# Optimization experiments

Hardware: AMD Instinct MI355X
Metric: run time of the kernel (lower is better)

Reference implementation:

```python
import jax, jax.numpy as jnp
import numpy as np

NODE_DIM = 128
EDGE_DIM = 128
N_NODES = 50000
N_EDGES = 600000


def setup_inputs() -> dict:
    key = jax.random.key(0)
    ks = jax.random.split(key, 10)
    d, e = NODE_DIM, EDGE_DIM
    s = lambda fan_in: 1.0 / np.sqrt(fan_in)
    return {
        "x": jax.random.normal(ks[0], (N_NODES, d), dtype=jnp.float32),
        "edge_index": jax.random.randint(ks[1], (2, N_EDGES), 0, N_NODES, dtype=jnp.int64),
        "edge_attr": jax.random.normal(ks[2], (N_EDGES, e), dtype=jnp.float32),
        # edge_net: Linear(2d+e -> 2d), Softplus, Linear(2d -> d), Softplus
        "W1": jax.random.uniform(ks[3], (2 * d + e, 2 * d), jnp.float32, -s(2 * d + e), s(2 * d + e)),
        "b1": jax.random.uniform(ks[4], (2 * d,), jnp.float32, -s(2 * d + e), s(2 * d + e)),
        "W2": jax.random.uniform(ks[5], (2 * d, d), jnp.float32, -s(2 * d), s(2 * d)),
        "b2": jax.random.uniform(ks[6], (d,), jnp.float32, -s(2 * d), s(2 * d)),
        # node_net: Linear(2d -> d), Softplus
        "Wn": jax.random.uniform(ks[7], (2 * d, d), jnp.float32, -s(2 * d), s(2 * d)),
        "bn": jax.random.uniform(ks[8], (d,), jnp.float32, -s(2 * d), s(2 * d)),
    }


def reference(x, edge_index, edge_attr, W1, b1, W2, b2, Wn, bn):
    row, col = edge_index[0], edge_index[1]
    # gather node features per edge and concat with edge features
    edge_input = jnp.concatenate([x[row], x[col], edge_attr], axis=-1)  # [E, 2d+e]
    h = jax.nn.softplus(edge_input @ W1 + b1)  # [E, 2d]
    edge_emb = jax.nn.softplus(h @ W2 + b2)    # [E, d]
    # scatter-add messages to destination nodes
    aggr = jax.ops.segment_sum(edge_emb, col, num_segments=x.shape[0])  # [N, d]
    node_input = jnp.concatenate([x, aggr], axis=-1)  # [N, 2d]
    x_new = jax.nn.softplus(node_input @ Wn + bn)     # [N, d]
    return x_new + x
```

## Files before the change

### kernel.cpp

```cpp
#include <hip/hip_runtime.h>

#define EE 600000
#define NN 50000
#define DD 128

typedef __bf16 bf16x8 __attribute__((ext_vector_type(8)));
typedef float f32x4 __attribute__((ext_vector_type(4)));
typedef unsigned short u16x8 __attribute__((ext_vector_type(8)));

__device__ inline unsigned short f2bf(float f) {
  unsigned int u = __builtin_bit_cast(unsigned int, f);
  u += 0x7FFFu + ((u >> 16) & 1u);
  return (unsigned short)(u >> 16);
}

__device__ inline float softplus_f(float v) {
  return fmaxf(v, 0.0f) + __logf(1.0f + __expf(-fabsf(v)));
}

__global__ void prep_kernel(const float* __restrict__ x,
                            const float* __restrict__ W1, const float* __restrict__ W2,
                            const float* __restrict__ Wn,
                            unsigned short* __restrict__ xbf, unsigned short* __restrict__ w1f,
                            unsigned short* __restrict__ w2f, unsigned short* __restrict__ wnf) {
  const int id = blockIdx.x * 256 + threadIdx.x;
  if (id < 800000) {
    const f32x4* src = (const f32x4*)(x + (size_t)id * 8);
    f32x4 f0 = src[0], f1 = src[1];
    u16x8 v;
#pragma unroll
    for (int j = 0; j < 4; ++j) { v[j] = f2bf(f0[j]); v[4 + j] = f2bf(f1[j]); }
    *(u16x8*)(xbf + (size_t)id * 8) = v;
  } else if (id < 812288) {
    const int u = id - 800000;
    const int l = u & 63, t2 = u >> 6, nt = t2 & 15, kt = t2 >> 4;
    const int n = nt * 16 + (l & 15);
    const int kb = kt * 32 + ((l >> 4) << 3);
    u16x8 v;
#pragma unroll
    for (int j = 0; j < 8; ++j) v[j] = f2bf(W1[(size_t)(kb + j) * 256 + n]);
    *(u16x8*)(w1f + (size_t)u * 8) = v;
  } else if (id < 816384) {
    const int u = id - 812288;
    const int l = u & 63, t2 = u >> 6, nt = t2 & 7, kt = t2 >> 3;
    const int n = nt * 16 + (l & 15);
    const int kb = kt * 32 + ((l >> 4) << 3);
    u16x8 v;
#pragma unroll
    for (int j = 0; j < 8; ++j) v[j] = f2bf(W2[(size_t)(kb + j) * 128 + n]);
    *(u16x8*)(w2f + (size_t)u * 8) = v;
  } else if (id < 820480) {
    const int u = id - 816384;
    const int l = u & 63, t2 = u >> 6, nt = t2 & 7, kt = t2 >> 3;
    const int n = nt * 16 + (l & 15);
    const int kb = kt * 32 + ((l >> 4) << 3);
    u16x8 v;
#pragma unroll
    for (int j = 0; j < 8; ++j) v[j] = f2bf(Wn[(size_t)(kb + j) * 128 + n]);
    *(u16x8*)(wnf + (size_t)u * 8) = v;
  }
}

__global__ __launch_bounds__(256, 3) void edge_kernel(
    const int* __restrict__ ei, const float* __restrict__ eattr,
    const float* __restrict__ b1, const float* __restrict__ b2,
    const unsigned short* __restrict__ xbf,
    const unsigned short* __restrict__ w1f, const unsigned short* __restrict__ w2f,
    float* __restrict__ aggr) {
  __shared__ __align__(16) unsigned short At[24576];
  __shared__ int colS[64];
  const int t = threadIdx.x;
  const int lane = t & 63;
  const int w = t >> 6;
  const int base = blockIdx.x * 64;

  {
    const int r = t >> 2, p = t & 3;
    const int e = base + r;
    const int sr = ei[e], sc = ei[EE + e];
    if (p == 0) colS[r] = sc;
    const u16x8* xr = (const u16x8*)(xbf + (size_t)sr * DD + p * 32);
    const u16x8* xc = (const u16x8*)(xbf + (size_t)sc * DD + p * 32);
    const f32x4* ea = (const f32x4*)(eattr + (size_t)e * DD + p * 32);
    const int swz = (r & 7) << 4;
    unsigned short* rowp = At + ((r * 768) >> 1);
#pragma unroll
    for (int i = 0; i < 4; ++i) {
      const int c2 = (p * 32 + i * 8) * 2;
      *(u16x8*)(rowp + ((c2 ^ swz) >> 1)) = xr[i];
      *(u16x8*)(rowp + (((256 + c2) ^ swz) >> 1)) = xc[i];
      f32x4 f0 = ea[2 * i], f1 = ea[2 * i + 1];
      u16x8 v;
#pragma unroll
      for (int j = 0; j < 4; ++j) { v[j] = f2bf(f0[j]); v[4 + j] = f2bf(f1[j]); }
      *(u16x8*)(rowp + (((512 + c2) ^ swz) >> 1)) = v;
    }
  }
  __syncthreads();

  const int lr = lane & 15;
  const int lkb = ((lane >> 4) << 3) * 2;

  f32x4 acc[4][4] = {};
#pragma unroll
  for (int kt = 0; kt < 12; ++kt) {
    bf16x8 a[4];
#pragma unroll
    for (int mt = 0; mt < 4; ++mt) {
      const int row = mt * 16 + lr;
      const int cb = kt * 64 + lkb;
      a[mt] = __builtin_bit_cast(bf16x8,
              *(const u16x8*)(At + ((row * 768 + (cb ^ ((row & 7) << 4))) >> 1)));
    }
#pragma unroll
    for (int nt = 0; nt < 4; ++nt) {
      const u16x8 bv = *(const u16x8*)(w1f + ((size_t)((kt * 16 + (w * 4 + nt)) * 64 + lane) << 3));
      const bf16x8 b = __builtin_bit_cast(bf16x8, bv);
#pragma unroll
      for (int mt = 0; mt < 4; ++mt)
        acc[mt][nt] = __builtin_amdgcn_mfma_f32_16x16x32_bf16(a[mt], b, acc[mt][nt], 0, 0, 0);
    }
  }
  __syncthreads();

#pragma unroll
  for (int nt = 0; nt < 4; ++nt) {
    const int col = w * 64 + nt * 16 + lr;
    const float bias = b1[col];
#pragma unroll
    for (int mt = 0; mt < 4; ++mt) {
#pragma unroll
      for (int reg = 0; reg < 4; ++reg) {
        const int row = mt * 16 + ((lane >> 4) << 2) + reg;
        const float hv = softplus_f(acc[mt][nt][reg] + bias);
        At[(row * 512 + ((col * 2) ^ ((row & 7) << 4))) >> 1] = f2bf(hv);
      }
    }
  }
  __syncthreads();

  f32x4 acc2[4][2] = {};
#pragma unroll
  for (int kt = 0; kt < 8; ++kt) {
    bf16x8 a[4];
#pragma unroll
    for (int mt = 0; mt < 4; ++mt) {
      const int row = mt * 16 + lr;
      const int cb = kt * 64 + lkb;
      a[mt] = __builtin_bit_cast(bf16x8,
              *(const u16x8*)(At + ((row * 512 + (cb ^ ((row & 7) << 4))) >> 1)));
    }
#pragma unroll
    for (int nt = 0; nt < 2; ++nt) {
      const u16x8 bv = *(const u16x8*)(w2f + ((size_t)((kt * 8 + (w * 2 + nt)) * 64 + lane) << 3));
      const bf16x8 b = __builtin_bit_cast(bf16x8, bv);
#pragma unroll
      for (int mt = 0; mt < 4; ++mt)
        acc2[mt][nt] = __builtin_amdgcn_mfma_f32_16x16x32_bf16(a[mt], b, acc2[mt][nt], 0, 0, 0);
    }
  }

#pragma unroll
  for (int nt = 0; nt < 2; ++nt) {
    const int col = w * 32 + nt * 16 + lr;
    const float bias = b2[col];
#pragma unroll
    for (int mt = 0; mt < 4; ++mt) {
#pragma unroll
      for (int reg = 0; reg < 4; ++reg) {
        const int row = mt * 16 + ((lane >> 4) << 2) + reg;
        const float v = softplus_f(acc2[mt][nt][reg] + bias);
        float* p = aggr + (size_t)colS[row] * DD + col;
        __hip_atomic_fetch_add(p, v, __ATOMIC_RELAXED, __HIP_MEMORY_SCOPE_AGENT);
      }
    }
  }
}

__global__ __launch_bounds__(256, 4) void node_kernel(
    const float* __restrict__ x, const float* __restrict__ bn,
    const unsigned short* __restrict__ xbf, const unsigned short* __restrict__ wnf,
    const float* __restrict__ aggr, float* __restrict__ out) {
  __shared__ __align__(16) unsigned short At[16384];
  const int t = threadIdx.x;
  const int lane = t & 63;
  const int w = t >> 6;
  const int base = blockIdx.x * 64;

  {
    const int r = t >> 2, p = t & 3;
    const int node = base + r;
    const int swz = (r & 7) << 4;
    unsigned short* rowp = At + ((r * 512) >> 1);
    if (node < NN) {
      const u16x8* xr = (const u16x8*)(xbf + (size_t)node * DD + p * 32);
      const f32x4* ag = (const f32x4*)(aggr + (size_t)node * DD + p * 32);
#pragma unroll
      for (int i = 0; i < 4; ++i) {
        const int c2 = (p * 32 + i * 8) * 2;
        *(u16x8*)(rowp + ((c2 ^ swz) >> 1)) = xr[i];
        f32x4 f0 = ag[2 * i], f1 = ag[2 * i + 1];
        u16x8 v;
#pragma unroll
        for (int j = 0; j < 4; ++j) { v[j] = f2bf(f0[j]); v[4 + j] = f2bf(f1[j]); }
        *(u16x8*)(rowp + (((256 + c2) ^ swz) >> 1)) = v;
      }
    } else {
      const u16x8 z = {};
#pragma unroll
      for (int i = 0; i < 4; ++i) {
        const int c2 = (p * 32 + i * 8) * 2;
        *(u16x8*)(rowp + ((c2 ^ swz) >> 1)) = z;
        *(u16x8*)(rowp + (((256 + c2) ^ swz) >> 1)) = z;
      }
    }
  }
  __syncthreads();

  const int lr = lane & 15;
  const int lkb = ((lane >> 4) << 3) * 2;
  f32x4 acc[4][2] = {};
#pragma unroll
  for (int kt = 0; kt < 8; ++kt) {
    bf16x8 a[4];
#pragma unroll
    for (int mt = 0; mt < 4; ++mt) {
      const int row = mt * 16 + lr;
      const int cb = kt * 64 + lkb;
      a[mt] = __builtin_bit_cast(bf16x8,
              *(const u16x8*)(At + ((row * 512 + (cb ^ ((row & 7) << 4))) >> 1)));
    }
#pragma unroll
    for (int nt = 0; nt < 2; ++nt) {
      const u16x8 bv = *(const u16x8*)(wnf + ((size_t)((kt * 8 + (w * 2 + nt)) * 64 + lane) << 3));
      const bf16x8 b = __builtin_bit_cast(bf16x8, bv);
#pragma unroll
      for (int mt = 0; mt < 4; ++mt)
        acc[mt][nt] = __builtin_amdgcn_mfma_f32_16x16x32_bf16(a[mt], b, acc[mt][nt], 0, 0, 0);
    }
  }

#pragma unroll
  for (int nt = 0; nt < 2; ++nt) {
    const int col = w * 32 + nt * 16 + lr;
    const float bias = bn[col];
#pragma unroll
    for (int mt = 0; mt < 4; ++mt) {
#pragma unroll
      for (int reg = 0; reg < 4; ++reg) {
        const int row = mt * 16 + ((lane >> 4) << 2) + reg;
        const int node = base + row;
        if (node < NN) {
          const size_t o = (size_t)node * DD + col;
          out[o] = softplus_f(acc[mt][nt][reg] + bias) + x[o];
        }
      }
    }
  }
}

extern "C" void kernel_launch(void* const* d_in, const int* in_sizes, int n_in,
                              void* d_out, int out_size, void* d_ws, size_t ws_size,
                              hipStream_t stream) {
  const float* x = (const float*)d_in[0];
  const int* ei = (const int*)d_in[1];
  const float* eattr = (const float*)d_in[2];
  const float* W1 = (const float*)d_in[3];
  const float* b1 = (const float*)d_in[4];
  const float* W2 = (const float*)d_in[5];
  const float* b2 = (const float*)d_in[6];
  const float* Wn = (const float*)d_in[7];
  const float* bn = (const float*)d_in[8];
  float* out = (float*)d_out;

  char* ws = (char*)d_ws;
  float* aggr = (float*)(ws);
  unsigned short* xbf = (unsigned short*)(ws + 25600000);
  unsigned short* w1f = (unsigned short*)(ws + 38400000);
  unsigned short* w2f = (unsigned short*)(ws + 38596608);
  unsigned short* wnf = (unsigned short*)(ws + 38662144);

  hipMemsetAsync(aggr, 0, (size_t)NN * DD * sizeof(float), stream);
  prep_kernel<<<3205, 256, 0, stream>>>(x, W1, W2, Wn, xbf, w1f, w2f, wnf);
  edge_kernel<<<9375, 256, 0, stream>>>(ei, eattr, b1, b2, xbf, w1f, w2f, aggr);
  node_kernel<<<782, 256, 0, stream>>>(x, bn, xbf, wnf, aggr, out);
}
```

Measured before the change: 761.4 us.

## Halve edge tile to 32 rows for higher occupancy and fold memset into prep

Each edge_kernel block now processes 32 edges instead of 64. This halves LDS use and accumulator registers, and launch bounds are raised to 6 blocks per CU so more waves can hide the gather and atomic latency. The aggr zeroing moves from hipMemsetAsync into extra threads of prep_kernel, which removes a separate operation. The cost is that each B (weight) fragment loaded from global memory now feeds half as many MFMAs, so weight traffic per edge doubles.

```diff
diff --git a/kernel.cpp b/kernel.cpp
--- a/kernel.cpp
+++ b/kernel.cpp
@@ -22,7 +22,8 @@
                             const float* __restrict__ W1, const float* __restrict__ W2,
                             const float* __restrict__ Wn,
                             unsigned short* __restrict__ xbf, unsigned short* __restrict__ w1f,
-                            unsigned short* __restrict__ w2f, unsigned short* __restrict__ wnf) {
+                            unsigned short* __restrict__ w2f, unsigned short* __restrict__ wnf,
+                            float* __restrict__ aggr) {
   const int id = blockIdx.x * 256 + threadIdx.x;
   if (id < 800000) {
     const f32x4* src = (const f32x4*)(x + (size_t)id * 8);
@@ -58,55 +59,59 @@
 #pragma unroll
     for (int j = 0; j < 8; ++j) v[j] = f2bf(Wn[(size_t)(kb + j) * 128 + n]);
     *(u16x8*)(wnf + (size_t)u * 8) = v;
-  }
-}
-
-__global__ __launch_bounds__(256, 3) void edge_kernel(
+  } else if (id < 2420480) {
+    const int u = id - 820480;
+    *(f32x4*)(aggr + (size_t)u * 4) = f32x4{0.f, 0.f, 0.f, 0.f};
+  }
+}
+
+__global__ __launch_bounds__(256, 6) void edge_kernel(
     const int* __restrict__ ei, const float* __restrict__ eattr,
     const float* __restrict__ b1, const float* __restrict__ b2,
     const unsigned short* __restrict__ xbf,
     const unsigned short* __restrict__ w1f, const unsigned short* __restrict__ w2f,
     float* __restrict__ aggr) {
-  __shared__ __align__(16) unsigned short At[24576];
-  __shared__ int colS[64];
+  __shared__ __align__(16) unsigned short At[12288];
+  __shared__ int colS[32];
   const int t = threadIdx.x;
   const int lane = t & 63;
   const int w = t >> 6;
-  const int base = blockIdx.x * 64;
+  const int base = blockIdx.x * 32;
 
   {
-    const int r = t >> 2, p = t & 3;
+    const int r = t >> 3, p = t & 7;
     const int e = base + r;
     const int sr = ei[e], sc = ei[EE + e];
     if (p == 0) colS[r] = sc;
-    const u16x8* xr = (const u16x8*)(xbf + (size_t)sr * DD + p * 32);
-    const u16x8* xc = (const u16x8*)(xbf + (size_t)sc * DD + p * 32);
-    const f32x4* ea = (const f32x4*)(eattr + (size_t)e * DD + p * 32);
+    const u16x8* xr = (const u16x8*)(xbf + (size_t)sr * DD);
+    const u16x8* xc = (const u16x8*)(xbf + (size_t)sc * DD);
+    const f32x4* ea = (const f32x4*)(eattr + (size_t)e * DD);
     const int swz = (r & 7) << 4;
-    unsigned short* rowp = At + ((r * 768) >> 1);
-#pragma unroll
-    for (int i = 0; i < 4; ++i) {
-      const int c2 = (p * 32 + i * 8) * 2;
-      *(u16x8*)(rowp + ((c2 ^ swz) >> 1)) = xr[i];
-      *(u16x8*)(rowp + (((256 + c2) ^ swz) >> 1)) = xc[i];
-      f32x4 f0 = ea[2 * i], f1 = ea[2 * i + 1];
+    unsigned short* rowp = At + r * 384;
+#pragma unroll
+    for (int i = 0; i < 2; ++i) {
+      const int c = 2 * p + i;
+      const int cb = c * 16;
+      *(u16x8*)(rowp + ((cb ^ swz) >> 1)) = xr[c];
+      *(u16x8*)(rowp + (((256 + cb) ^ swz) >> 1)) = xc[c];
+      f32x4 f0 = ea[2 * c], f1 = ea[2 * c + 1];
       u16x8 v;
 #pragma unroll
       for (int j = 0; j < 4; ++j) { v[j] = f2bf(f0[j]); v[4 + j] = f2bf(f1[j]); }
-      *(u16x8*)(rowp + (((512 + c2) ^ swz) >> 1)) = v;
+      *(u16x8*)(rowp + (((512 + cb) ^ swz) >> 1)) = v;
     }
   }
   __syncthreads();
 
   const int lr = lane & 15;
-  const int lkb = ((lane >> 4) << 3) * 2;
-
-  f32x4 acc[4][4] = {};
+  const int lkb = (lane >> 4) << 4;
+
+  f32x4 acc[2][4] = {};
 #pragma unroll
   for (int kt = 0; kt < 12; ++kt) {
-    bf16x8 a[4];
-#pragma unroll
-    for (int mt = 0; mt < 4; ++mt) {
+    bf16x8 a[2];
+#pragma unroll
+    for (int mt = 0; mt < 2; ++mt) {
       const int row = mt * 16 + lr;
       const int cb = kt * 64 + lkb;
       a[mt] = __builtin_bit_cast(bf16x8,
@@ -117,7 +122,7 @@
       const u16x8 bv = *(const u16x8*)(w1f + ((size_t)((kt * 16 + (w * 4 + nt)) * 64 + lane) << 3));
       const bf16x8 b = __builtin_bit_cast(bf16x8, bv);
 #pragma unroll
-      for (int mt = 0; mt < 4; ++mt)
+      for (int mt = 0; mt < 2; ++mt)
         acc[mt][nt] = __builtin_amdgcn_mfma_f32_16x16x32_bf16(a[mt], b, acc[mt][nt], 0, 0, 0);
     }
   }
@@ -128,7 +133,7 @@
     const int col = w * 64 + nt * 16 + lr;
     const float bias = b1[col];
 #pragma unroll
-    for (int mt = 0; mt < 4; ++mt) {
+    for (int mt = 0; mt < 2; ++mt) {
 #pragma unroll
       for (int reg = 0; reg < 4; ++reg) {
         const int row = mt * 16 + ((lane >> 4) << 2) + reg;
@@ -139,12 +144,12 @@
   }
   __syncthreads();
 
-  f32x4 acc2[4][2] = {};
+  f32x4 acc2[2][2] = {};
 #pragma unroll
   for (int kt = 0; kt < 8; ++kt) {
-    bf16x8 a[4];
-#pragma unroll
-    for (int mt = 0; mt < 4; ++mt) {
+    bf16x8 a[2];
+#pragma unroll
+    for (int mt = 0; mt < 2; ++mt) {
       const int row = mt * 16 + lr;
       const int cb = kt * 64 + lkb;
       a[mt] = __builtin_bit_cast(bf16x8,
@@ -155,7 +160,7 @@
       const u16x8 bv = *(const u16x8*)(w2f + ((size_t)((kt * 8 + (w * 2 + nt)) * 64 + lane) << 3));
       const bf16x8 b = __builtin_bit_cast(bf16x8, bv);
 #pragma unroll
-      for (int mt = 0; mt < 4; ++mt)
+      for (int mt = 0; mt < 2; ++mt)
         acc2[mt][nt] = __builtin_amdgcn_mfma_f32_16x16x32_bf16(a[mt], b, acc2[mt][nt], 0, 0, 0);
     }
   }
@@ -165,7 +170,7 @@
     const int col = w * 32 + nt * 16 + lr;
     const float bias = b2[col];
 #pragma unroll
-    for (int mt = 0; mt < 4; ++mt) {
+    for (int mt = 0; mt < 2; ++mt) {
 #pragma unroll
       for (int reg = 0; reg < 4; ++reg) {
         const int row = mt * 16 + ((lane >> 4) << 2) + reg;
@@ -218,7 +223,7 @@
   __syncthreads();
 
   const int lr = lane & 15;
-  const int lkb = ((lane >> 4) << 3) * 2;
+  const int lkb = (lane >> 4) << 4;
   f32x4 acc[4][2] = {};
 #pragma unroll
   for (int kt = 0; kt < 8; ++kt) {
@@ -280,8 +285,7 @@
   unsigned short* w2f = (unsigned short*)(ws + 38596608);
   unsigned short* wnf = (unsigned short*)(ws + 38662144);
 
-  hipMemsetAsync(aggr, 0, (size_t)NN * DD * sizeof(float), stream);
-  prep_kernel<<<3205, 256, 0, stream>>>(x, W1, W2, Wn, xbf, w1f, w2f, wnf);
-  edge_kernel<<<9375, 256, 0, stream>>>(ei, eattr, b1, b2, xbf, w1f, w2f, aggr);
+  prep_kernel<<<9455, 256, 0, stream>>>(x, W1, W2, Wn, xbf, w1f, w2f, wnf, aggr);
+  edge_kernel<<<18750, 256, 0, stream>>>(ei, eattr, b1, b2, xbf, w1f, w2f, aggr);
   node_kernel<<<782, 256, 0, stream>>>(x, bn, xbf, wnf, aggr, out);
 }
```

Measured after the change: 804.1 us. 1.06x slower.

## Pack column pairs into 64-bit fixed-point atomics for edge scatter-add

Applied to the files above, without the earlier changes.

Converts non-negative softplus edge messages to unsigned fixed-point, shuffles neighbour lanes to pack two columns per 64-bit word, and issues half as many integer atomic adds into the aggregate buffer. The node kernel decodes the fixed-point sums back to float. The zeroing memset is folded into the prep kernel. This trades precision and a bounded range per column sum (overflow would corrupt the neighbour column) for fewer, cheaper atomics.

```diff
diff --git a/kernel.cpp b/kernel.cpp
--- a/kernel.cpp
+++ b/kernel.cpp
@@ -3,6 +3,9 @@
 #define EE 600000
 #define NN 50000
 #define DD 128
+
+#define FXS 4194304.0f
+#define FXI 2.3841858e-07f
 
 typedef __bf16 bf16x8 __attribute__((ext_vector_type(8)));
 typedef float f32x4 __attribute__((ext_vector_type(4)));
@@ -22,7 +25,8 @@
                             const float* __restrict__ W1, const float* __restrict__ W2,
                             const float* __restrict__ Wn,
                             unsigned short* __restrict__ xbf, unsigned short* __restrict__ w1f,
-                            unsigned short* __restrict__ w2f, unsigned short* __restrict__ wnf) {
+                            unsigned short* __restrict__ w2f, unsigned short* __restrict__ wnf,
+                            float* __restrict__ aggr) {
   const int id = blockIdx.x * 256 + threadIdx.x;
   if (id < 800000) {
     const f32x4* src = (const f32x4*)(x + (size_t)id * 8);
@@ -58,6 +62,9 @@
 #pragma unroll
     for (int j = 0; j < 8; ++j) v[j] = f2bf(Wn[(size_t)(kb + j) * 128 + n]);
     *(u16x8*)(wnf + (size_t)u * 8) = v;
+  } else if (id < 2420480) {
+    const int u = id - 820480;
+    *(f32x4*)(aggr + (size_t)u * 4) = f32x4{0.f, 0.f, 0.f, 0.f};
   }
 }
 
@@ -66,7 +73,7 @@
     const float* __restrict__ b1, const float* __restrict__ b2,
     const unsigned short* __restrict__ xbf,
     const unsigned short* __restrict__ w1f, const unsigned short* __restrict__ w2f,
-    float* __restrict__ aggr) {
+    unsigned long long* __restrict__ aggr64) {
   __shared__ __align__(16) unsigned short At[24576];
   __shared__ int colS[64];
   const int t = threadIdx.x;
@@ -99,7 +106,7 @@
   __syncthreads();
 
   const int lr = lane & 15;
-  const int lkb = ((lane >> 4) << 3) * 2;
+  const int lkb = (lane >> 4) << 4;
 
   f32x4 acc[4][4] = {};
 #pragma unroll
@@ -160,19 +167,33 @@
     }
   }
 
+  const int parity = lane & 1;
 #pragma unroll
   for (int nt = 0; nt < 2; ++nt) {
     const int col = w * 32 + nt * 16 + lr;
     const float bias = b2[col];
-#pragma unroll
-    for (int mt = 0; mt < 4; ++mt) {
-#pragma unroll
-      for (int reg = 0; reg < 4; ++reg) {
-        const int row = mt * 16 + ((lane >> 4) << 2) + reg;
-        const float v = softplus_f(acc2[mt][nt][reg] + bias);
-        float* p = aggr + (size_t)colS[row] * DD + col;
-        __hip_atomic_fetch_add(p, v, __ATOMIC_RELAXED, __HIP_MEMORY_SCOPE_AGENT);
-      }
+    const int cp = col >> 1;
+#pragma unroll
+    for (int mt = 0; mt < 4; ++mt) {
+      const unsigned int fx0 = (unsigned int)(softplus_f(acc2[mt][nt][0] + bias) * FXS);
+      const unsigned int fx1 = (unsigned int)(softplus_f(acc2[mt][nt][1] + bias) * FXS);
+      const unsigned int fx2 = (unsigned int)(softplus_f(acc2[mt][nt][2] + bias) * FXS);
+      const unsigned int fx3 = (unsigned int)(softplus_f(acc2[mt][nt][3] + bias) * FXS);
+      const unsigned int sh0 = (unsigned int)__shfl_xor((int)fx0, 1);
+      const unsigned int sh1 = (unsigned int)__shfl_xor((int)fx1, 1);
+      const unsigned int sh2 = (unsigned int)__shfl_xor((int)fx2, 1);
+      const unsigned int sh3 = (unsigned int)__shfl_xor((int)fx3, 1);
+      const unsigned long long v0 = parity
+          ? (((unsigned long long)fx2 << 32) | sh2)
+          : (((unsigned long long)sh0 << 32) | fx0);
+      const unsigned long long v1 = parity
+          ? (((unsigned long long)fx3 << 32) | sh3)
+          : (((unsigned long long)sh1 << 32) | fx1);
+      const int rbase = mt * 16 + ((lane >> 4) << 2) + (parity << 1);
+      unsigned long long* p0 = aggr64 + (size_t)colS[rbase] * 64 + cp;
+      unsigned long long* p1 = aggr64 + (size_t)colS[rbase + 1] * 64 + cp;
+      __hip_atomic_fetch_add(p0, v0, __ATOMIC_RELAXED, __HIP_MEMORY_SCOPE_AGENT);
+      __hip_atomic_fetch_add(p1, v1, __ATOMIC_RELAXED, __HIP_MEMORY_SCOPE_AGENT);
     }
   }
 }
@@ -180,7 +201,7 @@
 __global__ __launch_bounds__(256, 4) void node_kernel(
     const float* __restrict__ x, const float* __restrict__ bn,
     const unsigned short* __restrict__ xbf, const unsigned short* __restrict__ wnf,
-    const float* __restrict__ aggr, float* __restrict__ out) {
+    const unsigned int* __restrict__ aggrU, float* __restrict__ out) {
   __shared__ __align__(16) unsigned short At[16384];
   const int t = threadIdx.x;
   const int lane = t & 63;
@@ -194,15 +215,17 @@
     unsigned short* rowp = At + ((r * 512) >> 1);
     if (node < NN) {
       const u16x8* xr = (const u16x8*)(xbf + (size_t)node * DD + p * 32);
-      const f32x4* ag = (const f32x4*)(aggr + (size_t)node * DD + p * 32);
+      const uint4* ag = (const uint4*)(aggrU + (size_t)node * DD + p * 32);
 #pragma unroll
       for (int i = 0; i < 4; ++i) {
         const int c2 = (p * 32 + i * 8) * 2;
         *(u16x8*)(rowp + ((c2 ^ swz) >> 1)) = xr[i];
-        f32x4 f0 = ag[2 * i], f1 = ag[2 * i + 1];
+        const uint4 q0 = ag[2 * i], q1 = ag[2 * i + 1];
         u16x8 v;
-#pragma unroll
-        for (int j = 0; j < 4; ++j) { v[j] = f2bf(f0[j]); v[4 + j] = f2bf(f1[j]); }
+        v[0] = f2bf((float)q0.x * FXI); v[1] = f2bf((float)q0.y * FXI);
+        v[2] = f2bf((float)q0.z * FXI); v[3] = f2bf((float)q0.w * FXI);
+        v[4] = f2bf((float)q1.x * FXI); v[5] = f2bf((float)q1.y * FXI);
+        v[6] = f2bf((float)q1.z * FXI); v[7] = f2bf((float)q1.w * FXI);
         *(u16x8*)(rowp + (((256 + c2) ^ swz) >> 1)) = v;
       }
     } else {
@@ -218,7 +241,7 @@
   __syncthreads();
 
   const int lr = lane & 15;
-  const int lkb = ((lane >> 4) << 3) * 2;
+  const int lkb = (lane >> 4) << 4;
   f32x4 acc[4][2] = {};
 #pragma unroll
   for (int kt = 0; kt < 8; ++kt) {
@@ -274,14 +297,15 @@
   float* out = (float*)d_out;
 
   char* ws = (char*)d_ws;
-  float* aggr = (float*)(ws);
+  float* aggrF = (float*)(ws);
+  unsigned long long* aggr64 = (unsigned long long*)(ws);
+  const unsigned int* aggrU = (const unsigned int*)(ws);
   unsigned short* xbf = (unsigned short*)(ws + 25600000);
   unsigned short* w1f = (unsigned short*)(ws + 38400000);
   unsigned short* w2f = (unsigned short*)(ws + 38596608);
   unsigned short* wnf = (unsigned short*)(ws + 38662144);
 
-  hipMemsetAsync(aggr, 0, (size_t)NN * DD * sizeof(float), stream);
-  prep_kernel<<<3205, 256, 0, stream>>>(x, W1, W2, Wn, xbf, w1f, w2f, wnf);
-  edge_kernel<<<9375, 256, 0, stream>>>(ei, eattr, b1, b2, xbf, w1f, w2f, aggr);
-  node_kernel<<<782, 256, 0, stream>>>(x, bn, xbf, wnf, aggr, out);
-}
+  prep_kernel<<<9455, 256, 0, stream>>>(x, W1, W2, Wn, xbf, w1f, w2f, wnf, aggrF);
+  edge_kernel<<<9375, 256, 0, stream>>>(ei, eattr, b1, b2, xbf, w1f, w2f, aggr64);
+  node_kernel<<<782, 256, 0, stream>>>(x, bn, xbf, wnf, aggrU, out);
+}
```

After: 756.8 us. Within noise of the previous version (-0.6%).

## Split edge layer-1 GEMM into three K-phases with prefetch and smaller LDS

Applied to the files above, without the earlier changes.

The edge kernel now stages the 64x384 input tile in three 128-column phases (x[row], x[col], edge_attr) through a 64x128 LDS buffer. The global load for the next phase is issued before the MFMA work of the current phase, so gather latency overlaps compute. The smaller LDS footprint lets launch bounds rise from 3 to 4 blocks per SM. The aggr memset is folded into the prep kernel to drop one launch, at the cost of extra syncs and register pressure from the prefetch buffers.

```diff
diff --git a/kernel.cpp b/kernel.cpp
--- a/kernel.cpp
+++ b/kernel.cpp
@@ -22,7 +22,8 @@
                             const float* __restrict__ W1, const float* __restrict__ W2,
                             const float* __restrict__ Wn,
                             unsigned short* __restrict__ xbf, unsigned short* __restrict__ w1f,
-                            unsigned short* __restrict__ w2f, unsigned short* __restrict__ wnf) {
+                            unsigned short* __restrict__ w2f, unsigned short* __restrict__ wnf,
+                            float* __restrict__ aggr) {
   const int id = blockIdx.x * 256 + threadIdx.x;
   if (id < 800000) {
     const f32x4* src = (const f32x4*)(x + (size_t)id * 8);
@@ -58,69 +59,106 @@
 #pragma unroll
     for (int j = 0; j < 8; ++j) v[j] = f2bf(Wn[(size_t)(kb + j) * 128 + n]);
     *(u16x8*)(wnf + (size_t)u * 8) = v;
-  }
-}
-
-__global__ __launch_bounds__(256, 3) void edge_kernel(
+  } else if (id < 2420480) {
+    const int u = id - 820480;
+    *(f32x4*)(aggr + (size_t)u * 4) = f32x4{0.f, 0.f, 0.f, 0.f};
+  }
+}
+
+__global__ __launch_bounds__(256, 4) void edge_kernel(
     const int* __restrict__ ei, const float* __restrict__ eattr,
     const float* __restrict__ b1, const float* __restrict__ b2,
     const unsigned short* __restrict__ xbf,
     const unsigned short* __restrict__ w1f, const unsigned short* __restrict__ w2f,
     float* __restrict__ aggr) {
-  __shared__ __align__(16) unsigned short At[24576];
+  __shared__ __align__(16) unsigned short At[16384];
   __shared__ int colS[64];
   const int t = threadIdx.x;
   const int lane = t & 63;
   const int w = t >> 6;
   const int base = blockIdx.x * 64;
 
-  {
-    const int r = t >> 2, p = t & 3;
-    const int e = base + r;
-    const int sr = ei[e], sc = ei[EE + e];
-    if (p == 0) colS[r] = sc;
-    const u16x8* xr = (const u16x8*)(xbf + (size_t)sr * DD + p * 32);
-    const u16x8* xc = (const u16x8*)(xbf + (size_t)sc * DD + p * 32);
-    const f32x4* ea = (const f32x4*)(eattr + (size_t)e * DD + p * 32);
-    const int swz = (r & 7) << 4;
-    unsigned short* rowp = At + ((r * 768) >> 1);
+  const int r = t >> 2, p = t & 3;
+  const int e = base + r;
+  const int sr = ei[e], sc = ei[EE + e];
+  if (p == 0) colS[r] = sc;
+  const int swz = (r & 7) << 4;
+  unsigned short* rowp = At + r * 128;
+  const int cbase = 64 * p;
+
+  const int lr = lane & 15;
+  const int lkb = (lane >> 4) << 4;
+
+  f32x4 acc[4][4] = {};
+
+  auto l1step = [&](int ph) {
+#pragma unroll
+    for (int kk = 0; kk < 4; ++kk) {
+      bf16x8 a[4];
+#pragma unroll
+      for (int mt = 0; mt < 4; ++mt) {
+        const int row = mt * 16 + lr;
+        const int cb = kk * 64 + lkb;
+        a[mt] = __builtin_bit_cast(bf16x8,
+                *(const u16x8*)(At + ((row * 256 + (cb ^ ((row & 7) << 4))) >> 1)));
+      }
+      const int kt = ph * 4 + kk;
+#pragma unroll
+      for (int nt = 0; nt < 4; ++nt) {
+        const u16x8 bv = *(const u16x8*)(w1f + ((size_t)((kt * 16 + (w * 4 + nt)) * 64 + lane) << 3));
+        const bf16x8 b = __builtin_bit_cast(bf16x8, bv);
+#pragma unroll
+        for (int mt = 0; mt < 4; ++mt)
+          acc[mt][nt] = __builtin_amdgcn_mfma_f32_16x16x32_bf16(a[mt], b, acc[mt][nt], 0, 0, 0);
+      }
+    }
+  };
+
+  {
+    const u16x8* src = (const u16x8*)(xbf + (size_t)sr * DD + p * 32);
+    const u16x8 c0 = src[0], c1 = src[1], c2 = src[2], c3 = src[3];
+    *(u16x8*)(rowp + (((cbase +  0) ^ swz) >> 1)) = c0;
+    *(u16x8*)(rowp + (((cbase + 16) ^ swz) >> 1)) = c1;
+    *(u16x8*)(rowp + (((cbase + 32) ^ swz) >> 1)) = c2;
+    *(u16x8*)(rowp + (((cbase + 48) ^ swz) >> 1)) = c3;
+  }
+  __syncthreads();
+  u16x8 pf0, pf1, pf2, pf3;
+  {
+    const u16x8* src = (const u16x8*)(xbf + (size_t)sc * DD + p * 32);
+    pf0 = src[0]; pf1 = src[1]; pf2 = src[2]; pf3 = src[3];
+  }
+  l1step(0);
+  __syncthreads();
+
+  *(u16x8*)(rowp + (((cbase +  0) ^ swz) >> 1)) = pf0;
+  *(u16x8*)(rowp + (((cbase + 16) ^ swz) >> 1)) = pf1;
+  *(u16x8*)(rowp + (((cbase + 32) ^ swz) >> 1)) = pf2;
+  *(u16x8*)(rowp + (((cbase + 48) ^ swz) >> 1)) = pf3;
+  __syncthreads();
+  f32x4 ef[8];
+  {
+    const f32x4* src = (const f32x4*)(eattr + (size_t)e * DD + p * 32);
+#pragma unroll
+    for (int i = 0; i < 8; ++i) ef[i] = src[i];
+  }
+  l1step(1);
+  __syncthreads();
+
+  {
 #pragma unroll
     for (int i = 0; i < 4; ++i) {
-      const int c2 = (p * 32 + i * 8) * 2;
-      *(u16x8*)(rowp + ((c2 ^ swz) >> 1)) = xr[i];
-      *(u16x8*)(rowp + (((256 + c2) ^ swz) >> 1)) = xc[i];
-      f32x4 f0 = ea[2 * i], f1 = ea[2 * i + 1];
-      u16x8 v;
-#pragma unroll
-      for (int j = 0; j < 4; ++j) { v[j] = f2bf(f0[j]); v[4 + j] = f2bf(f1[j]); }
-      *(u16x8*)(rowp + (((512 + c2) ^ swz) >> 1)) = v;
-    }
-  }
-  __syncthreads();
-
-  const int lr = lane & 15;
-  const int lkb = ((lane >> 4) << 3) * 2;
-
-  f32x4 acc[4][4] = {};
-#pragma unroll
-  for (int kt = 0; kt < 12; ++kt) {
-    bf16x8 a[4];
-#pragma unroll
-    for (int mt = 0; mt < 4; ++mt) {
-      const int row = mt * 16 + lr;
-      const int cb = kt * 64 + lkb;
-      a[mt] = __builtin_bit_cast(bf16x8,
-              *(const u16x8*)(At + ((row * 768 + (cb ^ ((row & 7) << 4))) >> 1)));
-    }
-#pragma unroll
-    for (int nt = 0; nt < 4; ++nt) {
-      const u16x8 bv = *(const u16x8*)(w1f + ((size_t)((kt * 16 + (w * 4 + nt)) * 64 + lane) << 3));
-      const bf16x8 b = __builtin_bit_cast(bf16x8, bv);
-#pragma unroll
-      for (int mt = 0; mt < 4; ++mt)
-        acc[mt][nt] = __builtin_amdgcn_mfma_f32_16x16x32_bf16(a[mt], b, acc[mt][nt], 0, 0, 0);
-    }
-  }
+      u16x8 c;
+#pragma unroll
+      for (int j = 0; j < 4; ++j) {
+        c[j] = f2bf(ef[2 * i][j]);
+        c[4 + j] = f2bf(ef[2 * i + 1][j]);
+      }
+      *(u16x8*)(rowp + (((cbase + 16 * i) ^ swz) >> 1)) = c;
+    }
+  }
+  __syncthreads();
+  l1step(2);
   __syncthreads();
 
 #pragma unroll
@@ -170,8 +208,8 @@
       for (int reg = 0; reg < 4; ++reg) {
         const int row = mt * 16 + ((lane >> 4) << 2) + reg;
         const float v = softplus_f(acc2[mt][nt][reg] + bias);
-        float* p = aggr + (size_t)colS[row] * DD + col;
-        __hip_atomic_fetch_add(p, v, __ATOMIC_RELAXED, __HIP_MEMORY_SCOPE_AGENT);
+        float* pa = aggr + (size_t)colS[row] * DD + col;
+        __hip_atomic_fetch_add(pa, v, __ATOMIC_RELAXED, __HIP_MEMORY_SCOPE_AGENT);
       }
     }
   }
@@ -218,7 +256,7 @@
   __syncthreads();
 
   const int lr = lane & 15;
-  const int lkb = ((lane >> 4) << 3) * 2;
+  const int lkb = (lane >> 4) << 4;
   f32x4 acc[4][2] = {};
 #pragma unroll
   for (int kt = 0; kt < 8; ++kt) {
@@ -280,8 +318,7 @@
   unsigned short* w2f = (unsigned short*)(ws + 38596608);
   unsigned short* wnf = (unsigned short*)(ws + 38662144);
 
-  hipMemsetAsync(aggr, 0, (size_t)NN * DD * sizeof(float), stream);
-  prep_kernel<<<3205, 256, 0, stream>>>(x, W1, W2, Wn, xbf, w1f, w2f, wnf);
+  prep_kernel<<<9455, 256, 0, stream>>>(x, W1, W2, Wn, xbf, w1f, w2f, wnf, aggr);
   edge_kernel<<<9375, 256, 0, stream>>>(ei, eattr, b1, b2, xbf, w1f, w2f, aggr);
   node_kernel<<<782, 256, 0, stream>>>(x, bn, xbf, wnf, aggr, out);
 }
```

Measured after the change: 849.3 us. +11.5%, slower.
